# Kernel optimization log

Measured on AMD Instinct MI355X. Metric: run time of the kernel, lower is better.

## Reference

```python
import jax, jax.numpy as jnp
import numpy as np

THITA = 0.0001

def conv1x1_relu(x, w, b):
    # x: [B,C_in,H,W], w: [C_out,C_in], b: [C_out]; 1x1 conv + bias + ReLU
    return jax.nn.relu(jnp.einsum('bchw,oc->bohw', x, w) + b[None, :, None, None])

def down4(x):
    # F.interpolate(x, scale_factor=0.25), mode='nearest': input idx = floor(i/0.25) = 4*i
    return x[:, :, ::4, ::4]

def up4(x):
    return jnp.repeat(jnp.repeat(x, 4, axis=2), 4, axis=3)

def setup_inputs() -> dict:
    key = jax.random.key(0)
    ks = jax.random.split(key, 16)
    B, C, H, W = 4, 64, 256, 256
    s = 1.0 / np.sqrt(C)
    inp = {
        'x1': jax.random.normal(ks[0], (B, 2 * C, H, W), jnp.float32),
        'x2': jax.random.normal(ks[1], (B, C, H, W), jnp.float32),
        'event': jax.random.normal(ks[2], (B, C, H, W), jnp.float32),
        # x_feature_extract: 3C->C then C->C
        'xw0': jax.random.normal(ks[3], (C, 3 * C), jnp.float32) * (1.0 / np.sqrt(3 * C)),
        'xb0': jax.random.normal(ks[4], (C,), jnp.float32) * 0.01,
        'xw1': jax.random.normal(ks[5], (C, C), jnp.float32) * s,
        'xb1': jax.random.normal(ks[6], (C,), jnp.float32) * 0.01,
        # event_feature_extract: C->C then C->C
        'ew0': jax.random.normal(ks[7], (C, C), jnp.float32) * s,
        'eb0': jax.random.normal(ks[8], (C,), jnp.float32) * 0.01,
        'ew1': jax.random.normal(ks[9], (C, C), jnp.float32) * s,
        'eb1': jax.random.normal(ks[10], (C,), jnp.float32) * 0.01,
        # query / key / value 1x1 convs
        'qw': jax.random.normal(ks[11], (C, C), jnp.float32) * s,
        'qb': jnp.zeros((C,), jnp.float32),
        'kw': jax.random.normal(ks[12], (C, C), jnp.float32) * s,
        'kb': jnp.zeros((C,), jnp.float32),
        'vw': jax.random.normal(ks[13], (C, C), jnp.float32) * s,
        'vb': jnp.zeros((C,), jnp.float32),
        'gamma': jax.random.normal(ks[14], (1,), jnp.float32),
    }
    return inp

def reference(x1, x2, event, xw0, xb0, xw1, xb1, ew0, eb0, ew1, eb1, qw, qb, kw, kb, vw, vb, gamma):
    x = jnp.concatenate([x1, x2], axis=1)                 # [B,3C,H,W]
    x = conv1x1_relu(x, xw0, xb0)                         # [B,C,H,W]
    ef = conv1x1_relu(event, ew0, eb0)                    # [B,C,H,W]
    x_2 = down4(x)                                        # [B,C,H/4,W/4]
    ef = down4(ef)
    x_2 = conv1x1_relu(x_2, xw1, xb1)
    ef = conv1x1_relu(ef, ew1, eb1)
    B, C, h, w = x_2.shape
    N = h * w
    q = conv1x1_relu(x_2, qw, qb).reshape(B, C, N)        # [B,C,N]
    k = conv1x1_relu(ef, kw, kb).reshape(B, C, N)         # [B,C,N]
    energy = jnp.einsum('bcn,bcm->bnm', q, k)             # [B,N,N]
    attention = jax.nn.softmax(energy, axis=-1)
    v = conv1x1_relu(x_2, vw, vb).reshape(B, C, N)        # [B,C,N]
    out = jnp.einsum('bcn,bmn->bcm', v, attention)        # bmm(v, att^T)
    out = out.reshape(B, C, h, w)
    out = up4(out)                                        # [B,C,H,W]
    out = gamma * out
    out = THITA * out + x
    ef_up = up4(ef)
    return (out, ef_up)
```

## Files before the change

kernel.cpp:

```cpp
#include <hip/hip_runtime.h>

typedef __attribute__((ext_vector_type(8))) short bf16x8;
typedef __attribute__((ext_vector_type(4))) float f32x4;

__device__ __forceinline__ unsigned pk2(float f0, float f1) {
  return __builtin_amdgcn_perm(__float_as_uint(f1) + 0x8000u,
                               __float_as_uint(f0) + 0x8000u, 0x07060302u);
}
__device__ __forceinline__ short f2bf_s(float f) {
  return (short)((__float_as_uint(f) + 0x8000u) >> 16);
}
__device__ __forceinline__ float bf2f(short s) {
  return __uint_as_float(((unsigned)(unsigned short)s) << 16);
}

__global__ __launch_bounds__(256, 3) void k1_conv192(
    const float* __restrict__ x1, const float* __restrict__ x2,
    const float* __restrict__ w0, const float* __restrict__ b0,
    float* __restrict__ xout, short* __restrict__ xds)
{
  const int b    = blockIdx.y;
  const int wv   = threadIdx.x >> 6;
  const int lane = threadIdx.x & 63;
  const int quad = lane >> 4;
  const int l16  = lane & 15;
  const int n0   = blockIdx.x * 256 + wv * 64;

  f32x4 acc[4][4];
  #pragma unroll
  for (int mt = 0; mt < 4; ++mt)
    #pragma unroll
    for (int nt = 0; nt < 4; ++nt)
      acc[mt][nt] = (f32x4){0.f, 0.f, 0.f, 0.f};

  #pragma unroll
  for (int kc = 0; kc < 6; ++kc) {
    bf16x8 af[4];
    #pragma unroll
    for (int mt = 0; mt < 4; ++mt) {
      const float* wrow = w0 + (mt * 16 + l16) * 192 + kc * 32 + quad * 8;
      float4 wa = *(const float4*)wrow;
      float4 wb = *(const float4*)(wrow + 4);
      union { unsigned i[4]; bf16x8 v; } u;
      u.i[0] = pk2(wa.x, wa.y); u.i[1] = pk2(wa.z, wa.w);
      u.i[2] = pk2(wb.x, wb.y); u.i[3] = pk2(wb.z, wb.w);
      af[mt] = u.v;
    }
    const float* src = (kc < 4)
        ? (x1 + ((long)b * 128 + kc * 32) * 65536)
        : (x2 + ((long)b * 64 + (kc - 4) * 32) * 65536);
    const float* s8 = src + (long)(quad * 8) * 65536;
    bf16x8 bfv[4];
    #pragma unroll
    for (int nt = 0; nt < 4; ++nt) {
      const int p = n0 + nt * 16 + l16;
      float e[8];
      #pragma unroll
      for (int j = 0; j < 8; ++j) e[j] = s8[(long)j * 65536 + p];
      union { unsigned i[4]; bf16x8 v; } u;
      #pragma unroll
      for (int j = 0; j < 4; ++j) u.i[j] = pk2(e[2 * j], e[2 * j + 1]);
      bfv[nt] = u.v;
    }
    #pragma unroll
    for (int mt = 0; mt < 4; ++mt)
      #pragma unroll
      for (int nt = 0; nt < 4; ++nt)
        acc[mt][nt] = __builtin_amdgcn_mfma_f32_16x16x32_bf16(
            af[mt], bfv[nt], acc[mt][nt], 0, 0, 0);
  }

  #pragma unroll
  for (int mt = 0; mt < 4; ++mt) {
    const float4 bb = *(const float4*)(b0 + mt * 16 + quad * 4);
    #pragma unroll
    for (int r = 0; r < 4; ++r) {
      const int o = mt * 16 + quad * 4 + r;
      const float bias = (r == 0) ? bb.x : (r == 1) ? bb.y : (r == 2) ? bb.z : bb.w;
      float* orow = xout + ((long)b * 64 + o) * 65536;
      #pragma unroll
      for (int nt = 0; nt < 4; ++nt)
        orow[n0 + nt * 16 + l16] = fmaxf(acc[mt][nt][r] + bias, 0.f);
    }
  }
  if (((blockIdx.x & 3) == 0) && ((l16 & 3) == 0)) {
    const int nbase = (blockIdx.x >> 2) * 64 + wv * 16 + (l16 >> 2);
    #pragma unroll
    for (int mt = 0; mt < 4; ++mt) {
      const float4 bb = *(const float4*)(b0 + mt * 16 + quad * 4);
      #pragma unroll
      for (int nt = 0; nt < 4; ++nt) {
        const float v0 = fmaxf(acc[mt][nt][0] + bb.x, 0.f);
        const float v1 = fmaxf(acc[mt][nt][1] + bb.y, 0.f);
        const float v2 = fmaxf(acc[mt][nt][2] + bb.z, 0.f);
        const float v3 = fmaxf(acc[mt][nt][3] + bb.w, 0.f);
        union { unsigned i[2]; unsigned long long q; } u;
        u.i[0] = pk2(v0, v1); u.i[1] = pk2(v2, v3);
        const int n = nbase + nt * 4;
        *(unsigned long long*)(xds + ((long)b * 4096 + n) * 64 + mt * 16 + quad * 4) = u.q;
      }
    }
  }
}

__device__ __forceinline__ void loadw_frag(const float* __restrict__ w,
                                           int row, int quad, bf16x8 wf[2]) {
  #pragma unroll
  for (int kc = 0; kc < 2; ++kc) {
    const float* p = w + row * 64 + kc * 32 + quad * 8;
    float4 a = *(const float4*)p;
    float4 c = *(const float4*)(p + 4);
    union { unsigned i[4]; bf16x8 v; } u;
    u.i[0] = pk2(a.x, a.y); u.i[1] = pk2(a.z, a.w);
    u.i[2] = pk2(c.x, c.y); u.i[3] = pk2(c.z, c.w);
    wf[kc] = u.v;
  }
}

__device__ __forceinline__ void conv_mfma(const short (*src)[72], short (*dst)[72],
                                          const bf16x8* wf,
                                          const float* __restrict__ bias,
                                          int ch0, int l16, int quad) {
  const float4 bv4 = *(const float4*)(bias + ch0);
  #pragma unroll
  for (int nt = 0; nt < 4; ++nt) {
    f32x4 acc = (f32x4){0.f, 0.f, 0.f, 0.f};
    #pragma unroll
    for (int kc = 0; kc < 2; ++kc) {
      bf16x8 bv = *(const bf16x8*)&src[nt * 16 + l16][kc * 32 + quad * 8];
      acc = __builtin_amdgcn_mfma_f32_16x16x32_bf16(wf[kc], bv, acc, 0, 0, 0);
    }
    const float v0 = fmaxf(acc[0] + bv4.x, 0.f);
    const float v1 = fmaxf(acc[1] + bv4.y, 0.f);
    const float v2 = fmaxf(acc[2] + bv4.z, 0.f);
    const float v3 = fmaxf(acc[3] + bv4.w, 0.f);
    union { unsigned i[2]; unsigned long long q; } u;
    u.i[0] = pk2(v0, v1); u.i[1] = pk2(v2, v3);
    *(unsigned long long*)&dst[nt * 16 + l16][ch0] = u.q;
  }
}

__global__ __launch_bounds__(256) void k2_small(
    const short* __restrict__ xds, const float* __restrict__ event,
    const float* __restrict__ xw1, const float* __restrict__ xb1,
    const float* __restrict__ ew0, const float* __restrict__ eb0,
    const float* __restrict__ ew1, const float* __restrict__ eb1,
    const float* __restrict__ qw, const float* __restrict__ qb,
    const float* __restrict__ kw, const float* __restrict__ kb,
    const float* __restrict__ vw, const float* __restrict__ vb,
    short* __restrict__ q_pm, short* __restrict__ k_pm,
    short* __restrict__ v_cm, short* __restrict__ ef_cm)
{
  __shared__ short A[64][72], Bb[64][72], Cb[64][72];
  const int b    = blockIdx.y;
  const int h4   = blockIdx.x;
  const int t    = threadIdx.x;
  const int lane = t & 63;
  const int g    = t >> 6;
  const int quad = lane >> 4;
  const int l16  = lane & 15;
  const int row  = g * 16 + l16;
  const int ch0  = g * 16 + quad * 4;

  bf16x8 wfx1[2], wfq[2], wfv[2], wfe0[2], wfe1[2], wfk[2];
  loadw_frag(xw1, row, quad, wfx1);
  loadw_frag(qw,  row, quad, wfq);
  loadw_frag(vw,  row, quad, wfv);
  loadw_frag(ew0, row, quad, wfe0);
  loadw_frag(ew1, row, quad, wfe1);
  loadw_frag(kw,  row, quad, wfk);

  const int px  = t >> 2;
  const int seg = t & 3;
  {
    const short* s = xds + ((long)b * 4096 + h4 * 64 + px) * 64 + seg * 16;
    *(bf16x8*)&A[px][seg * 16]     = *(const bf16x8*)s;
    *(bf16x8*)&A[px][seg * 16 + 8] = *(const bf16x8*)(s + 8);
  }
  __syncthreads();
  conv_mfma(A, Bb, wfx1, xb1, ch0, l16, quad);
  __syncthreads();
  conv_mfma(Bb, A,  wfq, qb, ch0, l16, quad);
  conv_mfma(Bb, Cb, wfv, vb, ch0, l16, quad);
  __syncthreads();
  {
    short* qdst = q_pm + ((long)b * 4096 + h4 * 64 + px) * 64 + seg * 16;
    *(bf16x8*)qdst       = *(const bf16x8*)&A[px][seg * 16];
    *(bf16x8*)(qdst + 8) = *(const bf16x8*)&A[px][seg * 16 + 8];
    union { short s[16]; int4 q2[2]; } vv;
    #pragma unroll
    for (int i = 0; i < 16; ++i) vv.s[i] = Cb[seg * 16 + i][px];
    int4* vdst = (int4*)(v_cm + ((long)b * 64 + px) * 4096 + h4 * 64 + seg * 16);
    vdst[0] = vv.q2[0]; vdst[1] = vv.q2[1];
    const int px2 = t & 63, cg = t >> 6;
    const float* ev = event + (long)b * 64 * 65536 + (long)h4 * 1024 + px2 * 4;
    #pragma unroll
    for (int r = 0; r < 16; r += 2) {
      const float e0v = ev[(long)(cg * 16 + r) * 65536];
      const float e1v = ev[(long)(cg * 16 + r + 1) * 65536];
      *(unsigned*)&Bb[px2][cg * 16 + r] = pk2(e0v, e1v);
    }
  }
  __syncthreads();
  conv_mfma(Bb, A,  wfe0, eb0, ch0, l16, quad);
  __syncthreads();
  conv_mfma(A,  Cb, wfe1, eb1, ch0, l16, quad);
  __syncthreads();
  conv_mfma(Cb, Bb, wfk, kb, ch0, l16, quad);
  {
    union { short s[16]; int4 q2[2]; } vv;
    #pragma unroll
    for (int i = 0; i < 16; ++i) vv.s[i] = Cb[seg * 16 + i][px];
    int4* edst = (int4*)(ef_cm + ((long)b * 64 + px) * 4096 + h4 * 64 + seg * 16);
    edst[0] = vv.q2[0]; edst[1] = vv.q2[1];
  }
  __syncthreads();
  {
    short* kdst = k_pm + ((long)b * 4096 + h4 * 64 + px) * 64 + seg * 16;
    *(bf16x8*)kdst       = *(const bf16x8*)&Bb[px][seg * 16];
    *(bf16x8*)(kdst + 8) = *(const bf16x8*)&Bb[px][seg * 16 + 8];
  }
}

__global__ __launch_bounds__(256) void k3_attn(
    const short* __restrict__ q_pm, const short* __restrict__ k_pm,
    const short* __restrict__ v_cm, short* __restrict__ O_pm)
{
  __shared__ short K_lds[64][72];
  __shared__ short V_lds[64][72];
  __shared__ short P_lds[4][16][72];
  const int b    = blockIdx.y;
  const int q0   = blockIdx.x * 64;
  const int t    = threadIdx.x;
  const int wv   = __builtin_amdgcn_readfirstlane(t >> 6);
  const int lane = t & 63;
  const int quad = lane >> 4;
  const int l16  = lane & 15;

  bf16x8 qf[2];
  {
    const short* qp = q_pm + ((long)b * 4096 + q0 + wv * 16 + l16) * 64 + quad * 8;
    qf[0] = *(const bf16x8*)(qp);
    qf[1] = *(const bf16x8*)(qp + 32);
  }
  f32x4 oacc[4];
  #pragma unroll
  for (int f = 0; f < 4; ++f) oacc[f] = (f32x4){0, 0, 0, 0};
  float run_m[4] = {-1e30f, -1e30f, -1e30f, -1e30f};
  float run_l[4] = {0, 0, 0, 0};

  const int kr  = t >> 2;
  const int seg = t & 3;
  const short* ksrc = k_pm + (long)b * 4096 * 64;
  const short* vsrc = v_cm + (long)b * 64 * 4096;

  for (int kt = 0; kt < 64; ++kt) {
    const int k0 = kt * 64;
    __syncthreads();
    {
      const short* s = ksrc + (long)(k0 + kr) * 64 + seg * 16;
      *(bf16x8*)&K_lds[kr][seg * 16]     = *(const bf16x8*)(s);
      *(bf16x8*)&K_lds[kr][seg * 16 + 8] = *(const bf16x8*)(s + 8);
      const short* v = vsrc + (long)kr * 4096 + k0 + seg * 16;
      *(bf16x8*)&V_lds[kr][seg * 16]     = *(const bf16x8*)(v);
      *(bf16x8*)&V_lds[kr][seg * 16 + 8] = *(const bf16x8*)(v + 8);
    }
    __syncthreads();

    f32x4 s[4];
    #pragma unroll
    for (int f = 0; f < 4; ++f) s[f] = (f32x4){0, 0, 0, 0};
    #pragma unroll
    for (int kc = 0; kc < 2; ++kc) {
      #pragma unroll
      for (int f = 0; f < 4; ++f) {
        bf16x8 bv = *(const bf16x8*)&K_lds[f * 16 + l16][kc * 32 + quad * 8];
        s[f] = __builtin_amdgcn_mfma_f32_16x16x32_bf16(qf[kc], bv, s[f], 0, 0, 0);
      }
    }
    float mrow[4], al[4], rs[4];
    #pragma unroll
    for (int r = 0; r < 4; ++r)
      mrow[r] = fmaxf(fmaxf(s[0][r], s[1][r]), fmaxf(s[2][r], s[3][r]));
    #pragma unroll
    for (int d = 1; d <= 8; d <<= 1)
      #pragma unroll
      for (int r = 0; r < 4; ++r)
        mrow[r] = fmaxf(mrow[r], __shfl_xor(mrow[r], d));
    #pragma unroll
    for (int r = 0; r < 4; ++r) {
      const float nm = fmaxf(run_m[r], mrow[r]);
      al[r] = __expf(run_m[r] - nm);
      run_m[r] = nm;
    }
    float pf[4][4];
    #pragma unroll
    for (int f = 0; f < 4; ++f)
      #pragma unroll
      for (int r = 0; r < 4; ++r)
        pf[f][r] = __expf(s[f][r] - run_m[r]);
    #pragma unroll
    for (int r = 0; r < 4; ++r)
      rs[r] = (pf[0][r] + pf[1][r]) + (pf[2][r] + pf[3][r]);
    #pragma unroll
    for (int d = 1; d <= 8; d <<= 1)
      #pragma unroll
      for (int r = 0; r < 4; ++r)
        rs[r] += __shfl_xor(rs[r], d);
    #pragma unroll
    for (int r = 0; r < 4; ++r) run_l[r] = run_l[r] * al[r] + rs[r];
    #pragma unroll
    for (int f = 0; f < 4; ++f)
      #pragma unroll
      for (int r = 0; r < 4; ++r)
        oacc[f][r] *= al[r];
    #pragma unroll
    for (int f = 0; f < 4; ++f)
      #pragma unroll
      for (int r = 0; r < 4; ++r)
        P_lds[wv][quad * 4 + r][f * 16 + l16] = f2bf_s(pf[f][r]);
    #pragma unroll
    for (int kc = 0; kc < 2; ++kc) {
      bf16x8 ap = *(const bf16x8*)&P_lds[wv][l16][kc * 32 + quad * 8];
      #pragma unroll
      for (int f = 0; f < 4; ++f) {
        bf16x8 bv = *(const bf16x8*)&V_lds[f * 16 + l16][kc * 32 + quad * 8];
        oacc[f] = __builtin_amdgcn_mfma_f32_16x16x32_bf16(ap, bv, oacc[f], 0, 0, 0);
      }
    }
  }
  #pragma unroll
  for (int r = 0; r < 4; ++r) {
    const float inv = 1.f / run_l[r];
    short* orow = O_pm + ((long)b * 4096 + q0 + wv * 16 + quad * 4 + r) * 64;
    #pragma unroll
    for (int f = 0; f < 4; ++f)
      orow[f * 16 + l16] = f2bf_s(oacc[f][r] * inv);
  }
}

__global__ __launch_bounds__(256) void k4_final(
    const short* __restrict__ O_pm, const short* __restrict__ ef_cm,
    const float* __restrict__ gamma, float* __restrict__ dout)
{
  const long idx = (long)blockIdx.x * 256 + threadIdx.x;
  const long e4 = idx * 4;
  const int hw = (int)(e4 & 65535);
  const int bc = (int)(e4 >> 16);
  const int h = hw >> 8, w0 = hw & 255;
  const int n = (h >> 2) * 64 + (w0 >> 2);
  const int b = bc >> 6, c = bc & 63;
  const float s = 1e-4f * gamma[0];
  const float ov = s * bf2f(O_pm[((long)b * 4096 + n) * 64 + c]);
  float4 xv = *(float4*)(dout + e4);
  xv.x += ov; xv.y += ov; xv.z += ov; xv.w += ov;
  *(float4*)(dout + e4) = xv;
  const float ef = bf2f(ef_cm[(long)bc * 4096 + n]);
  *(float4*)(dout + 16777216 + e4) = make_float4(ef, ef, ef, ef);
}

extern "C" void kernel_launch(void* const* d_in, const int* in_sizes, int n_in,
                              void* d_out, int out_size, void* d_ws, size_t ws_size,
                              hipStream_t stream)
{
  const float* x1    = (const float*)d_in[0];
  const float* x2    = (const float*)d_in[1];
  const float* event = (const float*)d_in[2];
  const float* xw0   = (const float*)d_in[3];
  const float* xb0   = (const float*)d_in[4];
  const float* xw1   = (const float*)d_in[5];
  const float* xb1   = (const float*)d_in[6];
  const float* ew0   = (const float*)d_in[7];
  const float* eb0   = (const float*)d_in[8];
  const float* ew1   = (const float*)d_in[9];
  const float* eb1   = (const float*)d_in[10];
  const float* qw    = (const float*)d_in[11];
  const float* qb    = (const float*)d_in[12];
  const float* kw    = (const float*)d_in[13];
  const float* kb    = (const float*)d_in[14];
  const float* vw    = (const float*)d_in[15];
  const float* vb    = (const float*)d_in[16];
  const float* gamma = (const float*)d_in[17];
  float* dout = (float*)d_out;

  char* ws = (char*)d_ws;
  short* q_pm  = (short*)(ws);
  short* k_pm  = (short*)(ws + (2u << 20));
  short* v_cm  = (short*)(ws + (4u << 20));
  short* ef_cm = (short*)(ws + (6u << 20));
  short* O_pm  = (short*)(ws + (8u << 20));
  short* xds   = (short*)(ws + (10u << 20));

  k1_conv192<<<dim3(256, 4), 256, 0, stream>>>(x1, x2, xw0, xb0, dout, xds);
  k2_small<<<dim3(64, 4), 256, 0, stream>>>(xds, event, xw1, xb1, ew0, eb0,
                                            ew1, eb1, qw, qb, kw, kb, vw, vb,
                                            q_pm, k_pm, v_cm, ef_cm);
  k3_attn<<<dim3(64, 4), 256, 0, stream>>>(q_pm, k_pm, v_cm, O_pm);
  k4_final<<<16384, 256, 0, stream>>>(O_pm, ef_cm, gamma, dout);
}
```

Baseline: 481.5 us.

## Split attention over key chunks with double-buffered LDS and merge partials in final kernel

The attention kernel now splits the 4096 keys into four chunks across a third grid dimension. The launch grows from 256 to 1024 blocks, which fills more of the GPU's compute units. Each block double-buffers K/V tiles through registers into a swizzled LDS layout and computes S transposed so the row softmax needs fewer shuffles. It writes unnormalized partial outputs plus per-row max and sum. A new small kernel computes the combine weights, and the final kernel merges the four partials. This adds extra global traffic for the partial outputs and one more kernel launch.

```diff
diff --git a/kernel.cpp b/kernel.cpp
--- a/kernel.cpp
+++ b/kernel.cpp
@@ -222,14 +222,16 @@
   }
 }
 
-__global__ __launch_bounds__(256) void k3_attn(
+__global__ __launch_bounds__(256, 4) void k3_attn(
     const short* __restrict__ q_pm, const short* __restrict__ k_pm,
-    const short* __restrict__ v_cm, short* __restrict__ O_pm)
-{
-  __shared__ short K_lds[64][72];
-  __shared__ short V_lds[64][72];
-  __shared__ short P_lds[4][16][72];
+    const short* __restrict__ v_cm, short* __restrict__ Opart,
+    float* __restrict__ ml)
+{
+  __shared__ short Kf[2][4096];
+  __shared__ short Vf[2][4096];
+  __shared__ short Pf[4][2][512];
   const int b    = blockIdx.y;
+  const int ks   = blockIdx.z;
   const int q0   = blockIdx.x * 64;
   const int t    = threadIdx.x;
   const int wv   = __builtin_amdgcn_readfirstlane(t >> 6);
@@ -240,108 +242,145 @@
   bf16x8 qf[2];
   {
     const short* qp = q_pm + ((long)b * 4096 + q0 + wv * 16 + l16) * 64 + quad * 8;
-    qf[0] = *(const bf16x8*)(qp);
+    qf[0] = *(const bf16x8*)qp;
     qf[1] = *(const bf16x8*)(qp + 32);
   }
+
+  const int srow  = t >> 2;
+  const int seg   = t & 3;
+  const int doff0 = (((seg >> 1) * 4 + (srow >> 4)) * 64 +
+                     ((seg & 1) * 2) * 16 + (srow & 15)) * 8;
+  const short* kbase = k_pm + (long)b * 4096 * 64;
+  const short* vbase = v_cm + (long)b * 64 * 4096;
+  const int kt0 = ks * 16;
+
+  bf16x8 krg[2], vrg[2];
+  {
+    const short* s = kbase + (long)(kt0 * 64 + srow) * 64 + seg * 16;
+    krg[0] = *(const bf16x8*)s; krg[1] = *(const bf16x8*)(s + 8);
+    const short* v = vbase + (long)srow * 4096 + kt0 * 64 + seg * 16;
+    vrg[0] = *(const bf16x8*)v; vrg[1] = *(const bf16x8*)(v + 8);
+  }
+  *(bf16x8*)&Kf[0][doff0]       = krg[0];
+  *(bf16x8*)&Kf[0][doff0 + 128] = krg[1];
+  *(bf16x8*)&Vf[0][doff0]       = vrg[0];
+  *(bf16x8*)&Vf[0][doff0 + 128] = vrg[1];
+  __syncthreads();
+
   f32x4 oacc[4];
   #pragma unroll
   for (int f = 0; f < 4; ++f) oacc[f] = (f32x4){0, 0, 0, 0};
-  float run_m[4] = {-1e30f, -1e30f, -1e30f, -1e30f};
-  float run_l[4] = {0, 0, 0, 0};
-
-  const int kr  = t >> 2;
-  const int seg = t & 3;
-  const short* ksrc = k_pm + (long)b * 4096 * 64;
-  const short* vsrc = v_cm + (long)b * 64 * 4096;
-
-  for (int kt = 0; kt < 64; ++kt) {
-    const int k0 = kt * 64;
-    __syncthreads();
-    {
-      const short* s = ksrc + (long)(k0 + kr) * 64 + seg * 16;
-      *(bf16x8*)&K_lds[kr][seg * 16]     = *(const bf16x8*)(s);
-      *(bf16x8*)&K_lds[kr][seg * 16 + 8] = *(const bf16x8*)(s + 8);
-      const short* v = vsrc + (long)kr * 4096 + k0 + seg * 16;
-      *(bf16x8*)&V_lds[kr][seg * 16]     = *(const bf16x8*)(v);
-      *(bf16x8*)&V_lds[kr][seg * 16 + 8] = *(const bf16x8*)(v + 8);
-    }
-    __syncthreads();
-
-    f32x4 s[4];
-    #pragma unroll
-    for (int f = 0; f < 4; ++f) s[f] = (f32x4){0, 0, 0, 0};
+  float run_m = -1e30f, run_l = 0.f;
+
+  for (int kt = 0; kt < 16; ++kt) {
+    if (kt < 15) {
+      const int k0 = (kt0 + kt + 1) * 64;
+      const short* s = kbase + (long)(k0 + srow) * 64 + seg * 16;
+      krg[0] = *(const bf16x8*)s; krg[1] = *(const bf16x8*)(s + 8);
+      const short* v = vbase + (long)srow * 4096 + k0 + seg * 16;
+      vrg[0] = *(const bf16x8*)v; vrg[1] = *(const bf16x8*)(v + 8);
+    }
+    const int buf = kt & 1;
+
+    f32x4 st[4];
+    #pragma unroll
+    for (int f = 0; f < 4; ++f) st[f] = (f32x4){0, 0, 0, 0};
+    #pragma unroll
+    for (int kc = 0; kc < 2; ++kc)
+      #pragma unroll
+      for (int f = 0; f < 4; ++f) {
+        bf16x8 ka = *(const bf16x8*)&Kf[buf][((kc * 4 + f) * 64 + lane) * 8];
+        st[f] = __builtin_amdgcn_mfma_f32_16x16x32_bf16(ka, qf[kc], st[f], 0, 0, 0);
+      }
+
+    float tm = st[0][0];
+    #pragma unroll
+    for (int f = 0; f < 4; ++f)
+      #pragma unroll
+      for (int r = 0; r < 4; ++r) tm = fmaxf(tm, st[f][r]);
+    tm = fmaxf(tm, __shfl_xor(tm, 16));
+    tm = fmaxf(tm, __shfl_xor(tm, 32));
+    const float nm = fmaxf(run_m, tm);
+    const float al = __expf(run_m - nm);
+    run_m = nm;
+    float pf[4][4], ts = 0.f;
+    #pragma unroll
+    for (int f = 0; f < 4; ++f)
+      #pragma unroll
+      for (int r = 0; r < 4; ++r) {
+        pf[f][r] = __expf(st[f][r] - nm);
+        ts += pf[f][r];
+      }
+    ts += __shfl_xor(ts, 16);
+    ts += __shfl_xor(ts, 32);
+    run_l = run_l * al + ts;
+    #pragma unroll
+    for (int f = 0; f < 4; ++f)
+      #pragma unroll
+      for (int r = 0; r < 4; ++r) oacc[f][r] *= al;
+
+    #pragma unroll
+    for (int f = 0; f < 4; ++f) {
+      union { unsigned i[2]; unsigned long long q; } u;
+      u.i[0] = pk2(pf[f][0], pf[f][1]);
+      u.i[1] = pk2(pf[f][2], pf[f][3]);
+      const int qd = (f & 1) * 2 + (quad >> 1);
+      *(unsigned long long*)&Pf[wv][f >> 1][(qd * 16 + l16) * 8 + (quad & 1) * 4] = u.q;
+    }
     #pragma unroll
     for (int kc = 0; kc < 2; ++kc) {
+      bf16x8 pb = *(const bf16x8*)&Pf[wv][kc][lane * 8];
       #pragma unroll
       for (int f = 0; f < 4; ++f) {
-        bf16x8 bv = *(const bf16x8*)&K_lds[f * 16 + l16][kc * 32 + quad * 8];
-        s[f] = __builtin_amdgcn_mfma_f32_16x16x32_bf16(qf[kc], bv, s[f], 0, 0, 0);
+        bf16x8 va = *(const bf16x8*)&Vf[buf][((kc * 4 + f) * 64 + lane) * 8];
+        oacc[f] = __builtin_amdgcn_mfma_f32_16x16x32_bf16(va, pb, oacc[f], 0, 0, 0);
       }
     }
-    float mrow[4], al[4], rs[4];
-    #pragma unroll
-    for (int r = 0; r < 4; ++r)
-      mrow[r] = fmaxf(fmaxf(s[0][r], s[1][r]), fmaxf(s[2][r], s[3][r]));
-    #pragma unroll
-    for (int d = 1; d <= 8; d <<= 1)
-      #pragma unroll
-      for (int r = 0; r < 4; ++r)
-        mrow[r] = fmaxf(mrow[r], __shfl_xor(mrow[r], d));
+
+    if (kt < 15) {
+      const int nb = buf ^ 1;
+      *(bf16x8*)&Kf[nb][doff0]       = krg[0];
+      *(bf16x8*)&Kf[nb][doff0 + 128] = krg[1];
+      *(bf16x8*)&Vf[nb][doff0]       = vrg[0];
+      *(bf16x8*)&Vf[nb][doff0 + 128] = vrg[1];
+      __syncthreads();
+    }
+  }
+
+  const int q = q0 + wv * 16 + l16;
+  #pragma unroll
+  for (int f = 0; f < 4; ++f)
     #pragma unroll
     for (int r = 0; r < 4; ++r) {
-      const float nm = fmaxf(run_m[r], mrow[r]);
-      al[r] = __expf(run_m[r] - nm);
-      run_m[r] = nm;
-    }
-    float pf[4][4];
-    #pragma unroll
-    for (int f = 0; f < 4; ++f)
-      #pragma unroll
-      for (int r = 0; r < 4; ++r)
-        pf[f][r] = __expf(s[f][r] - run_m[r]);
-    #pragma unroll
-    for (int r = 0; r < 4; ++r)
-      rs[r] = (pf[0][r] + pf[1][r]) + (pf[2][r] + pf[3][r]);
-    #pragma unroll
-    for (int d = 1; d <= 8; d <<= 1)
-      #pragma unroll
-      for (int r = 0; r < 4; ++r)
-        rs[r] += __shfl_xor(rs[r], d);
-    #pragma unroll
-    for (int r = 0; r < 4; ++r) run_l[r] = run_l[r] * al[r] + rs[r];
-    #pragma unroll
-    for (int f = 0; f < 4; ++f)
-      #pragma unroll
-      for (int r = 0; r < 4; ++r)
-        oacc[f][r] *= al[r];
-    #pragma unroll
-    for (int f = 0; f < 4; ++f)
-      #pragma unroll
-      for (int r = 0; r < 4; ++r)
-        P_lds[wv][quad * 4 + r][f * 16 + l16] = f2bf_s(pf[f][r]);
-    #pragma unroll
-    for (int kc = 0; kc < 2; ++kc) {
-      bf16x8 ap = *(const bf16x8*)&P_lds[wv][l16][kc * 32 + quad * 8];
-      #pragma unroll
-      for (int f = 0; f < 4; ++f) {
-        bf16x8 bv = *(const bf16x8*)&V_lds[f * 16 + l16][kc * 32 + quad * 8];
-        oacc[f] = __builtin_amdgcn_mfma_f32_16x16x32_bf16(ap, bv, oacc[f], 0, 0, 0);
-      }
-    }
-  }
-  #pragma unroll
-  for (int r = 0; r < 4; ++r) {
-    const float inv = 1.f / run_l[r];
-    short* orow = O_pm + ((long)b * 4096 + q0 + wv * 16 + quad * 4 + r) * 64;
-    #pragma unroll
-    for (int f = 0; f < 4; ++f)
-      orow[f * 16 + l16] = f2bf_s(oacc[f][r] * inv);
-  }
+      const int ch = f * 16 + quad * 4 + r;
+      Opart[((long)(ks * 4 + b) * 64 + ch) * 4096 + q] = f2bf_s(oacc[f][r]);
+    }
+  if (quad == 0) {
+    float2 v = make_float2(run_m, run_l);
+    *(float2*)&ml[((long)(ks * 4 + b) * 4096 + q) * 2] = v;
+  }
+}
+
+__global__ __launch_bounds__(256) void k3w(const float* __restrict__ ml,
+                                           float* __restrict__ wc)
+{
+  const int idx = blockIdx.x * 256 + threadIdx.x;
+  const float2* m2 = (const float2*)ml;
+  float2 s0 = m2[0 * 16384 + idx];
+  float2 s1 = m2[1 * 16384 + idx];
+  float2 s2 = m2[2 * 16384 + idx];
+  float2 s3 = m2[3 * 16384 + idx];
+  const float M = fmaxf(fmaxf(s0.x, s1.x), fmaxf(s2.x, s3.x));
+  const float e0 = __expf(s0.x - M), e1 = __expf(s1.x - M);
+  const float e2 = __expf(s2.x - M), e3 = __expf(s3.x - M);
+  const float inv = 1.f / (e0 * s0.y + e1 * s1.y + e2 * s2.y + e3 * s3.y);
+  *(float4*)&wc[idx * 4] = make_float4(e0 * inv, e1 * inv, e2 * inv, e3 * inv);
 }
 
 __global__ __launch_bounds__(256) void k4_final(
-    const short* __restrict__ O_pm, const short* __restrict__ ef_cm,
-    const float* __restrict__ gamma, float* __restrict__ dout)
+    const short* __restrict__ Opart, const float* __restrict__ wc,
+    const short* __restrict__ ef_cm, const float* __restrict__ gamma,
+    float* __restrict__ dout)
 {
   const long idx = (long)blockIdx.x * 256 + threadIdx.x;
   const long e4 = idx * 4;
@@ -351,7 +390,13 @@
   const int n = (h >> 2) * 64 + (w0 >> 2);
   const int b = bc >> 6, c = bc & 63;
   const float s = 1e-4f * gamma[0];
-  const float ov = s * bf2f(O_pm[((long)b * 4096 + n) * 64 + c]);
+  const float4 w4 = *(const float4*)&wc[((long)b * 4096 + n) * 4];
+  const long obase = ((long)b * 64 + c) * 4096 + n;
+  float ov = w4.x * bf2f(Opart[obase]) +
+             w4.y * bf2f(Opart[obase + (long)1 * 4 * 64 * 4096]) +
+             w4.z * bf2f(Opart[obase + (long)2 * 4 * 64 * 4096]) +
+             w4.w * bf2f(Opart[obase + (long)3 * 4 * 64 * 4096]);
+  ov *= s;
   float4 xv = *(float4*)(dout + e4);
   xv.x += ov; xv.y += ov; xv.z += ov; xv.w += ov;
   *(float4*)(dout + e4) = xv;
@@ -388,13 +433,16 @@
   short* k_pm  = (short*)(ws + (2u << 20));
   short* v_cm  = (short*)(ws + (4u << 20));
   short* ef_cm = (short*)(ws + (6u << 20));
-  short* O_pm  = (short*)(ws + (8u << 20));
-  short* xds   = (short*)(ws + (10u << 20));
+  short* xds   = (short*)(ws + (8u << 20));
+  short* Opart = (short*)(ws + (10u << 20));
+  float* ml    = (float*)(ws + (18u << 20));
+  float* wc    = (float*)(ws + (18u << 20) + (512u << 10));
 
   k1_conv192<<<dim3(256, 4), 256, 0, stream>>>(x1, x2, xw0, xb0, dout, xds);
   k2_small<<<dim3(64, 4), 256, 0, stream>>>(xds, event, xw1, xb1, ew0, eb0,
                                             ew1, eb1, qw, qb, kw, kb, vw, vb,
                                             q_pm, k_pm, v_cm, ef_cm);
-  k3_attn<<<dim3(64, 4), 256, 0, stream>>>(q_pm, k_pm, v_cm, O_pm);
-  k4_final<<<16384, 256, 0, stream>>>(O_pm, ef_cm, gamma, dout);
-}
+  k3_attn<<<dim3(64, 4, 4), 256, 0, stream>>>(q_pm, k_pm, v_cm, Opart, ml);
+  k3w<<<64, 256, 0, stream>>>(ml, wc);
+  k4_final<<<16384, 256, 0, stream>>>(Opart, wc, ef_cm, gamma, dout);
+}
```

Result: faster. 421.1 us (-12.5%).
